# Kernel tuning notes

Measured on AMD Instinct MI355X. Metric: run time of the kernel, lower is better.

Reference implementation:

```python
import jax, jax.numpy as jnp
import numpy as np
from math import pi

H = 1024        # hidden_size
CAP = 32        # capacity (even -> CAP//2 even+odd rotation pairs)
EH = H // 2         # even_hidden_size = 512
OH = (H - 1) // 2   # odd_hidden_size  = 511
PAIRS = CAP // 2    # 16

# fixed permutations (hidden_size even branch of the original module)
_PE = np.arange(H).reshape(-1, 2)[:, ::-1].reshape(-1)                       # swap (0,1),(2,3),...
_inner = np.arange(1, 2 * OH + 1).reshape(-1, 2)[:, ::-1].reshape(-1)
_PO = np.concatenate([[0], _inner, [2 * OH + 1]])                            # fix ends, swap interior pairs


def cm(x, y):
    """complex multiply; real/imag stacked in last dim."""
    xr, xi = x[..., 0], x[..., 1]
    yr, yi = y[..., 0], y[..., 1]
    return jnp.stack([xr * yr - xi * yi, xr * yi + xi * yr], -1)


def _ilv(a, b):
    """interleave two [n] vectors -> [2n]."""
    return jnp.stack([a, b], 1).reshape(-1)


def setup_inputs() -> dict:
    key = jax.random.key(0)
    ks = jax.random.split(key, 6)
    u = lambda k, shape: jax.random.uniform(k, shape, jnp.float32) * (2 * pi) - pi
    return {
        "x": jax.random.normal(ks[0], (4096, H, 2), jnp.float32),
        "omega": u(ks[1], (H,)),
        "even_theta": u(ks[2], (PAIRS, EH)),
        "odd_theta": u(ks[3], (PAIRS, OH)),
        "even_phi": u(ks[4], (PAIRS, EH)),
        "odd_phi": u(ks[5], (PAIRS, OH)),
    }


def reference(x, omega, even_theta, odd_theta, even_phi, odd_phi):
    PE = jnp.asarray(_PE)
    PO = jnp.asarray(_PO)

    def step(xc, p):
        et, ep, ot, op = p
        # ---- even rotation (note: original code swaps cos_phi/sin_phi in the
        # call to _v_diag/_v_off_diag; replicated faithfully here) ----
        ct, st, cp, sp = jnp.cos(et), jnp.sin(et), jnp.cos(ep), jnp.sin(ep)
        z = jnp.zeros_like(ct)
        vd = jnp.stack([_ilv(sp * ct, ct), _ilv(cp * ct, z)], -1)          # [H,2]
        vo = jnp.stack([_ilv(-sp * st, st), _ilv(-cp * st, z)], -1)        # [H,2]
        xc = cm(xc, vd) + cm(xc[:, PE, :], vo)
        # ---- odd rotation (ends padded with identity) ----
        ct, st, cp, sp = jnp.cos(ot), jnp.sin(ot), jnp.cos(op), jnp.sin(op)
        z = jnp.zeros_like(ct)
        one = jnp.ones((1,), xc.dtype)
        zero = jnp.zeros((1,), xc.dtype)
        vd_re = jnp.concatenate([one, _ilv(sp * ct, ct), one])
        vd_im = jnp.concatenate([zero, _ilv(cp * ct, z), zero])
        vo_re = jnp.concatenate([zero, _ilv(-sp * st, st), zero])
        vo_im = jnp.concatenate([zero, _ilv(-cp * st, z), zero])
        xc = cm(xc, jnp.stack([vd_re, vd_im], -1)) + cm(xc[:, PO, :], jnp.stack([vo_re, vo_im], -1))
        return xc, None

    x, _ = jax.lax.scan(step, x, (even_theta, even_phi, odd_theta, odd_phi))
    # final diagonal phase
    x = cm(x, jnp.stack([jnp.cos(omega), jnp.sin(omega)], -1))
    return x
```

## Files before the change

### kernel.cpp

```cpp
#include <hip/hip_runtime.h>
#include <math.h>


typedef float f4 __attribute__((ext_vector_type(4)));

#define OMCS_OFF 65536

__global__ __launch_bounds__(256) void eunn_precompute(
    const float* __restrict__ omega, const float* __restrict__ et,
    const float* __restrict__ ot, const float* __restrict__ ep,
    const float* __restrict__ op, float* __restrict__ ws) {
  int tid = blockIdx.x * 256 + threadIdx.x;
  if (tid < 16384) {
    int s = tid >> 10, k = tid & 1023;
    int phase = k >> 9, j = k & 511;
    float ct, st, cp, sp;
    if (phase == 0) {
      sincosf(et[s * 512 + j], &st, &ct);
      sincosf(ep[s * 512 + j], &sp, &cp);
    } else if (j < 511) {
      sincosf(ot[s * 511 + j], &st, &ct);
      sincosf(op[s * 511 + j], &sp, &cp);
    } else {
      ct = 1.f; st = 0.f; cp = 0.f; sp = 1.f;
    }
    ((f4*)ws)[s * 1024 + phase * 512 + (j & 7) * 64 + (j >> 3)] =
        (f4){ct, st, cp, sp};
  } else if (tid < 16896) {
    int m = tid - 16384;
    float s0, c0, s1, c1;
    sincosf(omega[2 * m], &s0, &c0);
    sincosf(omega[2 * m + 1], &s1, &c1);
    ((f4*)(ws + OMCS_OFF))[(m & 7) * 64 + (m >> 3)] = (f4){c0, s0, c1, s1};
  }
}

template <int R>
__global__ __launch_bounds__(256, 2) void eunn_main(
    const float* __restrict__ x, float* __restrict__ out,
    const float* __restrict__ ws) {
  __shared__ f4 cbuf[2][1024];
  const int tid = threadIdx.x;
  const int lane = tid & 63;
  const int wid = blockIdx.x * (blockDim.x >> 6) + (tid >> 6);
  const f4* wsf = (const f4*)ws;

  f4 p0 = wsf[tid], p1 = wsf[tid + 256], p2 = wsf[tid + 512], p3 = wsf[tid + 768];

  f4 e[R][8];
#pragma unroll
  for (int r = 0; r < R; ++r) {
    const f4* xr = (const f4*)(x + (size_t)(wid * R + r) * 2048) + lane * 8;
#pragma unroll
    for (int p = 0; p < 8; ++p) e[r][p] = xr[p];
  }

  cbuf[0][tid] = p0;
  cbuf[0][tid + 256] = p1;
  cbuf[0][tid + 512] = p2;
  cbuf[0][tid + 768] = p3;
  __syncthreads();

#pragma unroll 1
  for (int s = 0; s < 16; ++s) {
    const int cur = s & 1, nxt = cur ^ 1;
    const f4* nb = wsf + ((s + 1) & 15) * 1024;
    f4 n0 = nb[tid], n1 = nb[tid + 256], n2 = nb[tid + 512], n3 = nb[tid + 768];

    f4 E[8], O[8];
#pragma unroll
    for (int p = 0; p < 8; ++p) E[p] = cbuf[cur][p * 64 + lane];
#pragma unroll
    for (int p = 0; p < 8; ++p) O[p] = cbuf[cur][512 + p * 64 + lane];

#pragma unroll
    for (int r = 0; r < R; ++r) {
#pragma unroll
      for (int p = 0; p < 8; ++p) {
        f4 c = E[p];
        f4 v = e[r][p];
        float t0 = c.x * v.x - c.y * v.z;
        float t1 = c.x * v.y - c.y * v.w;
        e[r][p] = (f4){c.w * t0 - c.z * t1, c.z * t0 + c.w * t1,
                       c.y * v.x + c.x * v.z, c.y * v.y + c.x * v.w};
      }
    }

    {
      float ctm = __shfl_up(O[7].x, 1, 64);
      float stm = __shfl_up(O[7].y, 1, 64);
      if (lane == 0) { ctm = 1.f; stm = 0.f; }
#pragma unroll
      for (int r = 0; r < R; ++r) {
        float upx = __shfl_down(e[r][0].x, 1, 64);
        float upy = __shfl_down(e[r][0].y, 1, 64);
        float dnz = __shfl_up(e[r][7].z, 1, 64);
        float dnw = __shfl_up(e[r][7].w, 1, 64);
        float nx = stm * dnz + ctm * e[r][0].x;
        float ny = stm * dnw + ctm * e[r][0].y;
        e[r][0].x = nx;
        e[r][0].y = ny;
#pragma unroll
        for (int p = 0; p < 7; ++p) {
          f4 c = O[p];
          float e0r = e[r][p].z, e0i = e[r][p].w;
          float e1r = e[r][p + 1].x, e1i = e[r][p + 1].y;
          float t0 = c.x * e0r - c.y * e1r;
          float t1 = c.x * e0i - c.y * e1i;
          e[r][p].z = c.w * t0 - c.z * t1;
          e[r][p].w = c.z * t0 + c.w * t1;
          e[r][p + 1].x = c.y * e0r + c.x * e1r;
          e[r][p + 1].y = c.y * e0i + c.x * e1i;
        }
        {
          f4 c = O[7];
          float e0r = e[r][7].z, e0i = e[r][7].w;
          float t0 = c.x * e0r - c.y * upx;
          float t1 = c.x * e0i - c.y * upy;
          e[r][7].z = c.w * t0 - c.z * t1;
          e[r][7].w = c.z * t0 + c.w * t1;
        }
      }
    }

    cbuf[nxt][tid] = n0;
    cbuf[nxt][tid + 256] = n1;
    cbuf[nxt][tid + 512] = n2;
    cbuf[nxt][tid + 768] = n3;
    __syncthreads();
  }

  const f4* om4 = (const f4*)(ws + OMCS_OFF) + lane;
#pragma unroll
  for (int r = 0; r < R; ++r) {
    f4* outr = (f4*)(out + (size_t)(wid * R + r) * 2048) + lane * 8;
#pragma unroll
    for (int p = 0; p < 8; ++p) {
      f4 v = e[r][p];
      f4 w = om4[p * 64];
      outr[p] = (f4){v.x * w.x - v.y * w.y, v.x * w.y + v.y * w.x,
                     v.z * w.z - v.w * w.w, v.z * w.w + v.w * w.z};
    }
  }
}

extern "C" void kernel_launch(void* const* d_in, const int* in_sizes, int n_in,
                              void* d_out, int out_size, void* d_ws, size_t ws_size,
                              hipStream_t stream) {
  const float* x     = (const float*)d_in[0];
  const float* omega = (const float*)d_in[1];
  const float* et    = (const float*)d_in[2];
  const float* ot    = (const float*)d_in[3];
  const float* ep    = (const float*)d_in[4];
  const float* op    = (const float*)d_in[5];
  float* out = (float*)d_out;
  float* ws  = (float*)d_ws;

  eunn_precompute<<<dim3(66), dim3(256), 0, stream>>>(omega, et, ot, ep, op, ws);

  eunn_main<2><<<dim3(512), dim3(256), 0, stream>>>(x, out, ws);
}
```

Measured before the change: 130.0 us.

## Fuse trig precompute into main kernel using hardware sin/cos per block

Removes the separate precompute launch. Each block now loads raw angles for the next stage, evaluates sin/cos with the hardware transcendental instructions, and writes them into the double-buffered LDS coefficient table. Rows per wave drop from two to one and occupancy is raised to four blocks per CU, which doubles the grid to 1024 blocks. This saves a kernel launch and the workspace round trip, at the cost of redundant trig work in every block and lower-precision hardware sin/cos with no range reduction.

Result: slower. 147.6 us (+13.6%).

```diff
diff --git a/kernel.cpp b/kernel.cpp
--- a/kernel.cpp
+++ b/kernel.cpp
@@ -3,69 +3,67 @@
 
 
 typedef float f4 __attribute__((ext_vector_type(4)));
+typedef float f2 __attribute__((ext_vector_type(2)));
 
-#define OMCS_OFF 65536
+#define INV_2PI 0.15915494309189535f
 
-__global__ __launch_bounds__(256) void eunn_precompute(
+__device__ __forceinline__ void hw_sc(float x, float* s, float* c) {
+  float r = x * INV_2PI;
+  *s = __builtin_amdgcn_sinf(r);
+  *c = __builtin_amdgcn_cosf(r);
+}
+
+__global__ __launch_bounds__(256, 4) void eunn_fused(
+    const float* __restrict__ x, float* __restrict__ out,
     const float* __restrict__ omega, const float* __restrict__ et,
     const float* __restrict__ ot, const float* __restrict__ ep,
-    const float* __restrict__ op, float* __restrict__ ws) {
-  int tid = blockIdx.x * 256 + threadIdx.x;
-  if (tid < 16384) {
-    int s = tid >> 10, k = tid & 1023;
-    int phase = k >> 9, j = k & 511;
+    const float* __restrict__ op) {
+  __shared__ f4 cbuf[2][1024];
+  const int tid = threadIdx.x;
+  const int lane = tid & 63;
+  const int row = blockIdx.x * 4 + (tid >> 6);
+  const int j0 = 2 * tid;
+
+  float let0, let1, lep0, lep1, lot0, lot1, lop0, lop1;
+  auto stage_load = [&](int s) {
+    f2 a = *(const f2*)(et + s * 512 + j0); let0 = a.x; let1 = a.y;
+    f2 b = *(const f2*)(ep + s * 512 + j0); lep0 = b.x; lep1 = b.y;
+    const float* otr = ot + s * 511;
+    const float* opr = op + s * 511;
+    lot0 = otr[j0]; lop0 = opr[j0];
+    if (j0 + 1 < 511) { lot1 = otr[j0 + 1]; lop1 = opr[j0 + 1]; }
+    else { lot1 = 0.f; lop1 = 0.f; }
+  };
+  auto stage_commit = [&](int b) {
     float ct, st, cp, sp;
-    if (phase == 0) {
-      sincosf(et[s * 512 + j], &st, &ct);
-      sincosf(ep[s * 512 + j], &sp, &cp);
-    } else if (j < 511) {
-      sincosf(ot[s * 511 + j], &st, &ct);
-      sincosf(op[s * 511 + j], &sp, &cp);
+    hw_sc(let0, &st, &ct); hw_sc(lep0, &sp, &cp);
+    cbuf[b][(j0 & 7) * 64 + (j0 >> 3)] = (f4){ct, st, cp, sp};
+    hw_sc(let1, &st, &ct); hw_sc(lep1, &sp, &cp);
+    cbuf[b][((j0 + 1) & 7) * 64 + ((j0 + 1) >> 3)] = (f4){ct, st, cp, sp};
+    hw_sc(lot0, &st, &ct); hw_sc(lop0, &sp, &cp);
+    cbuf[b][512 + (j0 & 7) * 64 + (j0 >> 3)] = (f4){ct, st, cp, sp};
+    if (j0 + 1 < 511) {
+      hw_sc(lot1, &st, &ct); hw_sc(lop1, &sp, &cp);
     } else {
       ct = 1.f; st = 0.f; cp = 0.f; sp = 1.f;
     }
-    ((f4*)ws)[s * 1024 + phase * 512 + (j & 7) * 64 + (j >> 3)] =
-        (f4){ct, st, cp, sp};
-  } else if (tid < 16896) {
-    int m = tid - 16384;
-    float s0, c0, s1, c1;
-    sincosf(omega[2 * m], &s0, &c0);
-    sincosf(omega[2 * m + 1], &s1, &c1);
-    ((f4*)(ws + OMCS_OFF))[(m & 7) * 64 + (m >> 3)] = (f4){c0, s0, c1, s1};
+    cbuf[b][512 + ((j0 + 1) & 7) * 64 + ((j0 + 1) >> 3)] = (f4){ct, st, cp, sp};
+  };
+
+  stage_load(0);
+  f4 e[8];
+  {
+    const f4* xr = (const f4*)(x + (size_t)row * 2048) + lane * 8;
+#pragma unroll
+    for (int p = 0; p < 8; ++p) e[p] = xr[p];
   }
-}
-
-template <int R>
-__global__ __launch_bounds__(256, 2) void eunn_main(
-    const float* __restrict__ x, float* __restrict__ out,
-    const float* __restrict__ ws) {
-  __shared__ f4 cbuf[2][1024];
-  const int tid = threadIdx.x;
-  const int lane = tid & 63;
-  const int wid = blockIdx.x * (blockDim.x >> 6) + (tid >> 6);
-  const f4* wsf = (const f4*)ws;
-
-  f4 p0 = wsf[tid], p1 = wsf[tid + 256], p2 = wsf[tid + 512], p3 = wsf[tid + 768];
-
-  f4 e[R][8];
-#pragma unroll
-  for (int r = 0; r < R; ++r) {
-    const f4* xr = (const f4*)(x + (size_t)(wid * R + r) * 2048) + lane * 8;
-#pragma unroll
-    for (int p = 0; p < 8; ++p) e[r][p] = xr[p];
-  }
-
-  cbuf[0][tid] = p0;
-  cbuf[0][tid + 256] = p1;
-  cbuf[0][tid + 512] = p2;
-  cbuf[0][tid + 768] = p3;
+  stage_commit(0);
   __syncthreads();
 
 #pragma unroll 1
   for (int s = 0; s < 16; ++s) {
-    const int cur = s & 1, nxt = cur ^ 1;
-    const f4* nb = wsf + ((s + 1) & 15) * 1024;
-    f4 n0 = nb[tid], n1 = nb[tid + 256], n2 = nb[tid + 512], n3 = nb[tid + 768];
+    const int cur = s & 1;
+    if (s < 15) stage_load(s + 1);
 
     f4 E[8], O[8];
 #pragma unroll
@@ -74,72 +72,71 @@
     for (int p = 0; p < 8; ++p) O[p] = cbuf[cur][512 + p * 64 + lane];
 
 #pragma unroll
-    for (int r = 0; r < R; ++r) {
-#pragma unroll
-      for (int p = 0; p < 8; ++p) {
-        f4 c = E[p];
-        f4 v = e[r][p];
-        float t0 = c.x * v.x - c.y * v.z;
-        float t1 = c.x * v.y - c.y * v.w;
-        e[r][p] = (f4){c.w * t0 - c.z * t1, c.z * t0 + c.w * t1,
-                       c.y * v.x + c.x * v.z, c.y * v.y + c.x * v.w};
-      }
+    for (int p = 0; p < 8; ++p) {
+      f4 c = E[p];
+      f4 v = e[p];
+      float t0 = c.x * v.x - c.y * v.z;
+      float t1 = c.x * v.y - c.y * v.w;
+      e[p] = (f4){c.w * t0 - c.z * t1, c.z * t0 + c.w * t1,
+                  c.y * v.x + c.x * v.z, c.y * v.y + c.x * v.w};
     }
 
     {
       float ctm = __shfl_up(O[7].x, 1, 64);
       float stm = __shfl_up(O[7].y, 1, 64);
       if (lane == 0) { ctm = 1.f; stm = 0.f; }
+      float upx = __shfl_down(e[0].x, 1, 64);
+      float upy = __shfl_down(e[0].y, 1, 64);
+      float dnz = __shfl_up(e[7].z, 1, 64);
+      float dnw = __shfl_up(e[7].w, 1, 64);
+      float nx = stm * dnz + ctm * e[0].x;
+      float ny = stm * dnw + ctm * e[0].y;
+      e[0].x = nx;
+      e[0].y = ny;
 #pragma unroll
-      for (int r = 0; r < R; ++r) {
-        float upx = __shfl_down(e[r][0].x, 1, 64);
-        float upy = __shfl_down(e[r][0].y, 1, 64);
-        float dnz = __shfl_up(e[r][7].z, 1, 64);
-        float dnw = __shfl_up(e[r][7].w, 1, 64);
-        float nx = stm * dnz + ctm * e[r][0].x;
-        float ny = stm * dnw + ctm * e[r][0].y;
-        e[r][0].x = nx;
-        e[r][0].y = ny;
-#pragma unroll
-        for (int p = 0; p < 7; ++p) {
-          f4 c = O[p];
-          float e0r = e[r][p].z, e0i = e[r][p].w;
-          float e1r = e[r][p + 1].x, e1i = e[r][p + 1].y;
-          float t0 = c.x * e0r - c.y * e1r;
-          float t1 = c.x * e0i - c.y * e1i;
-          e[r][p].z = c.w * t0 - c.z * t1;
-          e[r][p].w = c.z * t0 + c.w * t1;
-          e[r][p + 1].x = c.y * e0r + c.x * e1r;
-          e[r][p + 1].y = c.y * e0i + c.x * e1i;
-        }
-        {
-          f4 c = O[7];
-          float e0r = e[r][7].z, e0i = e[r][7].w;
-          float t0 = c.x * e0r - c.y * upx;
-          float t1 = c.x * e0i - c.y * upy;
-          e[r][7].z = c.w * t0 - c.z * t1;
-          e[r][7].w = c.z * t0 + c.w * t1;
-        }
+      for (int p = 0; p < 7; ++p) {
+        f4 c = O[p];
+        float e0r = e[p].z, e0i = e[p].w;
+        float e1r = e[p + 1].x, e1i = e[p + 1].y;
+        float t0 = c.x * e0r - c.y * e1r;
+        float t1 = c.x * e0i - c.y * e1i;
+        e[p].z = c.w * t0 - c.z * t1;
+        e[p].w = c.z * t0 + c.w * t1;
+        e[p + 1].x = c.y * e0r + c.x * e1r;
+        e[p + 1].y = c.y * e0i + c.x * e1i;
+      }
+      {
+        f4 c = O[7];
+        float e0r = e[7].z, e0i = e[7].w;
+        float t0 = c.x * e0r - c.y * upx;
+        float t1 = c.x * e0i - c.y * upy;
+        e[7].z = c.w * t0 - c.z * t1;
+        e[7].w = c.z * t0 + c.w * t1;
       }
     }
 
-    cbuf[nxt][tid] = n0;
-    cbuf[nxt][tid + 256] = n1;
-    cbuf[nxt][tid + 512] = n2;
-    cbuf[nxt][tid + 768] = n3;
-    __syncthreads();
+    if (s < 15) {
+      stage_commit(cur ^ 1);
+      __syncthreads();
+    }
   }
 
-  const f4* om4 = (const f4*)(ws + OMCS_OFF) + lane;
+  {
+    const float* omr = omega + lane * 16;
+    f4 og[4];
 #pragma unroll
-  for (int r = 0; r < R; ++r) {
-    f4* outr = (f4*)(out + (size_t)(wid * R + r) * 2048) + lane * 8;
+    for (int q = 0; q < 4; ++q) og[q] = *(const f4*)(omr + 4 * q);
+    f4* outr = (f4*)(out + (size_t)row * 2048) + lane * 8;
 #pragma unroll
     for (int p = 0; p < 8; ++p) {
-      f4 v = e[r][p];
-      f4 w = om4[p * 64];
-      outr[p] = (f4){v.x * w.x - v.y * w.y, v.x * w.y + v.y * w.x,
-                     v.z * w.z - v.w * w.w, v.z * w.w + v.w * w.z};
+      float w0 = og[p >> 1][(p & 1) * 2];
+      float w1 = og[p >> 1][(p & 1) * 2 + 1];
+      float c0, s0, c1, s1;
+      hw_sc(w0, &s0, &c0);
+      hw_sc(w1, &s1, &c1);
+      f4 v = e[p];
+      outr[p] = (f4){v.x * c0 - v.y * s0, v.x * s0 + v.y * c0,
+                     v.z * c1 - v.w * s1, v.z * s1 + v.w * c1};
     }
   }
 }
@@ -154,9 +151,6 @@
   const float* ep    = (const float*)d_in[4];
   const float* op    = (const float*)d_in[5];
   float* out = (float*)d_out;
-  float* ws  = (float*)d_ws;
 
-  eunn_precompute<<<dim3(66), dim3(256), 0, stream>>>(omega, et, ot, ep, op, ws);
-
-  eunn_main<2><<<dim3(512), dim3(256), 0, stream>>>(x, out, ws);
+  eunn_fused<<<dim3(1024), dim3(256), 0, stream>>>(x, out, omega, et, ot, ep, op);
 }
```
